# Optimization experiments

Measured on AMD Instinct MI355X. Metric: run time of the kernel, lower is better.

Reference implementation:

```python
import jax, jax.numpy as jnp
import numpy as np

D_MODEL = 2048
NUM_HEADS = 16
D_K = D_MODEL // NUM_HEADS
B, S = 2, 2048


def setup_inputs() -> dict:
    key = jax.random.key(0)
    ks = jax.random.split(key, 9)
    sc = 1.0 / np.sqrt(D_MODEL)
    x = jax.random.normal(ks[0], (B, S, D_MODEL), dtype=jnp.float32)
    # broadcastable causal mask [1,1,S,S]; mask==0 positions get -inf
    mask = jnp.tril(jnp.ones((S, S), dtype=jnp.int32))[None, None]
    wq = jax.random.normal(ks[1], (D_MODEL, D_MODEL), dtype=jnp.float32) * sc
    bq = jax.random.normal(ks[2], (D_MODEL,), dtype=jnp.float32) * 0.01
    wk = jax.random.normal(ks[3], (D_MODEL, D_MODEL), dtype=jnp.float32) * sc
    bk = jax.random.normal(ks[4], (D_MODEL,), dtype=jnp.float32) * 0.01
    wv = jax.random.normal(ks[5], (D_MODEL, D_MODEL), dtype=jnp.float32) * sc
    bv = jax.random.normal(ks[6], (D_MODEL,), dtype=jnp.float32) * 0.01
    wo = jax.random.normal(ks[7], (D_MODEL, D_MODEL), dtype=jnp.float32) * sc
    bo = jax.random.normal(ks[8], (D_MODEL,), dtype=jnp.float32) * 0.01
    return {"x": x, "wq": wq, "bq": bq, "wk": wk, "bk": bk,
            "wv": wv, "bv": bv, "wo": wo, "bo": bo, "mask": mask}


def reference(x, wq, bq, wk, bk, wv, bv, wo, bo, mask):
    b, s, _ = x.shape
    # nn.Linear computes x @ W.T + b; weights stored [out, in]
    def proj(w, bias):
        y = jnp.einsum('bsd,ed->bse', x, w) + bias
        return y.reshape(b, s, NUM_HEADS, D_K).transpose(0, 2, 1, 3)  # [b,h,s,dk]
    q = proj(wq, bq)
    k = proj(wk, bk)
    v = proj(wv, bv)
    scores = jnp.einsum('bhid,bhjd->bhij', q, k) / jnp.sqrt(jnp.float32(D_K))
    scores = jnp.where(mask == 0, -jnp.inf, scores)
    attn = jax.nn.softmax(scores, axis=-1)  # dropout p=0.0 -> identity
    out = jnp.einsum('bhij,bhjd->bhid', attn, v)
    out = out.transpose(0, 2, 1, 3).reshape(b, s, D_MODEL)
    return jnp.einsum('bsd,ed->bse', out, wo) + bo
```

## Files before the change

### kernel.cpp

```cpp
#include <hip/hip_runtime.h>
#include <cstdint>
#include <cstddef>

typedef __attribute__((ext_vector_type(8))) short bf16x8;
typedef __attribute__((ext_vector_type(8))) unsigned short u16x8;
typedef __attribute__((ext_vector_type(4))) unsigned short u16x4;
typedef __attribute__((ext_vector_type(4))) float f32x4;

#define MFMA16(A, B, C) __builtin_amdgcn_mfma_f32_16x16x32_bf16((A), (B), (C), 0, 0, 0)

__device__ __forceinline__ unsigned short f2bf(float f) {
  unsigned u = __builtin_bit_cast(unsigned, f);
  u += 0x7FFFu + ((u >> 16) & 1u);
  return (unsigned short)(u >> 16);
}

__device__ __forceinline__ void gload_lds16(const void* gsrc, void* ldst) {
  __builtin_amdgcn_global_load_lds(
      (const __attribute__((address_space(1))) unsigned int*)gsrc,
      (__attribute__((address_space(3))) unsigned int*)ldst,
      16, 0, 0);
}

__global__ __launch_bounds__(256) void cvt_all(
    const float* __restrict__ sx, const float* __restrict__ s1,
    const float* __restrict__ s2, const float* __restrict__ s3,
    const float* __restrict__ s4,
    unsigned short* __restrict__ dx, unsigned short* __restrict__ d1,
    unsigned short* __restrict__ d2, unsigned short* __restrict__ d3,
    unsigned short* __restrict__ d4) {
  const int y = blockIdx.y;
  const float* src;
  unsigned short* dst;
  if (y == 0)      { src = sx;               dst = dx; }
  else if (y == 1) { src = sx + (1u << 22);  dst = dx + (1u << 22); }
  else if (y == 2) { src = s1; dst = d1; }
  else if (y == 3) { src = s2; dst = d2; }
  else if (y == 4) { src = s3; dst = d3; }
  else             { src = s4; dst = d4; }
  const size_t i = ((size_t)blockIdx.x * 256 + threadIdx.x) * 4;
  f32x4 v = *(const f32x4*)(src + i);
  u16x4 o;
  o[0] = f2bf(v[0]); o[1] = f2bf(v[1]); o[2] = f2bf(v[2]); o[3] = f2bf(v[3]);
  *(u16x4*)(dst + i) = o;
}

template <int MODE>
__device__ __forceinline__ void gemm_tile(const unsigned short* __restrict__ A,
                                          const unsigned short* __restrict__ W,
                                          const float* __restrict__ bias,
                                          void* __restrict__ C,
                                          int bx, int by) {
  constexpr int K = 2048, N = 2048;
  __shared__ unsigned short lA[128 * 32];
  __shared__ unsigned short lB[128 * 32];
  const int tid = threadIdx.x;
  const int lane = tid & 63;
  const int w = tid >> 6;
  const int g = lane >> 4;
  const int l15 = lane & 15;
  const int wr = w >> 1, wc = w & 1;
  const int m0 = by * 128, n0 = bx * 128;

  f32x4 acc[4][4];
#pragma unroll
  for (int i = 0; i < 4; ++i)
#pragma unroll
    for (int j = 0; j < 4; ++j) acc[i][j] = f32x4{0.f, 0.f, 0.f, 0.f};

  for (int kt = 0; kt < K / 32; ++kt) {
    __syncthreads();
    const int kb = kt * 32;
#pragma unroll
    for (int it = 0; it < 2; ++it) {
      const int f = it * 256 + tid;
      const int r = f >> 2, s = f & 3;
      char* dA = (char*)lA + (it * 256 + w * 64) * 16;
      char* dB = (char*)lB + (it * 256 + w * 64) * 16;
      gload_lds16(A + (size_t)(m0 + r) * K + kb + s * 8, dA);
      gload_lds16(W + (size_t)(n0 + r) * K + kb + s * 8, dB);
    }
    __syncthreads();
    bf16x8 af[4], bfr[4];
#pragma unroll
    for (int mi = 0; mi < 4; ++mi)
      af[mi] = *(const bf16x8*)&lA[(wr * 64 + mi * 16 + l15) * 32 + g * 8];
#pragma unroll
    for (int ni = 0; ni < 4; ++ni)
      bfr[ni] = *(const bf16x8*)&lB[(wc * 64 + ni * 16 + l15) * 32 + g * 8];
#pragma unroll
    for (int mi = 0; mi < 4; ++mi)
#pragma unroll
      for (int ni = 0; ni < 4; ++ni)
        acc[mi][ni] = MFMA16(af[mi], bfr[ni], acc[mi][ni]);
  }

#pragma unroll
  for (int ni = 0; ni < 4; ++ni) {
    const int n = n0 + wc * 64 + ni * 16 + l15;
    const float bval = bias[n];
#pragma unroll
    for (int mi = 0; mi < 4; ++mi) {
      const int mb = m0 + wr * 64 + mi * 16 + g * 4;
#pragma unroll
      for (int r = 0; r < 4; ++r) {
        const int m = mb + r;
        const float fv = acc[mi][ni][r] + bval;
        if (MODE == 0) {
          ((float*)C)[(size_t)m * N + n] = fv;
        } else {
          const int bb = m >> 11, ss = m & 2047, hh = n >> 7, dk = n & 127;
          ((unsigned short*)C)[(((size_t)(bb * 16 + hh) * 2048) + ss) * 128 + dk] =
              f2bf(fv);
        }
      }
    }
  }
}

__global__ __launch_bounds__(256) void gemm_qkv(
    const unsigned short* __restrict__ x,
    const unsigned short* __restrict__ wq, const float* __restrict__ bq,
    const unsigned short* __restrict__ wk, const float* __restrict__ bk,
    const unsigned short* __restrict__ wv, const float* __restrict__ bv,
    unsigned short* __restrict__ qo, unsigned short* __restrict__ ko,
    unsigned short* __restrict__ vo) {
  const int z = blockIdx.z;
  const unsigned short* W = (z == 0) ? wq : (z == 1) ? wk : wv;
  const float* B = (z == 0) ? bq : (z == 1) ? bk : bv;
  unsigned short* O = (z == 0) ? qo : (z == 1) ? ko : vo;
  gemm_tile<1>(x, W, B, O, blockIdx.x, blockIdx.y);
}

__global__ __launch_bounds__(256) void gemm_out(
    const unsigned short* __restrict__ A, const unsigned short* __restrict__ wo,
    const float* __restrict__ bo, float* __restrict__ C) {
  gemm_tile<0>(A, wo, bo, C, blockIdx.x, blockIdx.y);
}

__global__ __launch_bounds__(256, 2) void attn_fwd(
    const unsigned short* __restrict__ Q, const unsigned short* __restrict__ K,
    const unsigned short* __restrict__ V, unsigned short* __restrict__ O) {
  __shared__ unsigned short lK[2][64 * 128];
  __shared__ unsigned short lV[128 * 72];
  __shared__ unsigned short lP[4][32 * 72];
  const int tid = threadIdx.x;
  const int lane = tid & 63;
  const int w = tid >> 6;
  const int g = lane >> 4;
  const int l15 = lane & 15;
  const int bx = blockIdx.x;
  const int bh = blockIdx.y;
  const int qb = (bh >= 16) ? (15 - bx) : bx;
  const int nt = 2 * qb + 2;
  const size_t head_off = (size_t)bh * 2048 * 128;
  const unsigned short* Qh = Q + head_off;
  const unsigned short* Kh = K + head_off;
  const unsigned short* Vh = V + head_off;

  bf16x8 qf[2][4];
#pragma unroll
  for (int mi = 0; mi < 2; ++mi) {
    const int row = qb * 128 + w * 32 + mi * 16 + l15;
#pragma unroll
    for (int ks = 0; ks < 4; ++ks) {
      const int s = ks * 4 + g;
      qf[mi][ks] = *(const bf16x8*)(Qh + (size_t)row * 128 + s * 8);
    }
  }

  const int vj0 = (tid & 31) * 2;
  const int vd0 = (tid >> 5) * 16;
  u16x8 vr[4];

  auto stageK = [&](int t, int buf) {
#pragma unroll
    for (int it = 0; it < 4; ++it) {
      const int f = it * 256 + tid;
      const int r = f >> 4, s = f & 15;
      const int sc = s ^ (r & 7);
      gload_lds16(Kh + (size_t)(t * 64 + r) * 128 + sc * 8,
                  (char*)&lK[buf][0] + (it * 256 + w * 64) * 16);
    }
  };
  auto loadV = [&](int t) {
    const unsigned short* vp = Vh + (size_t)(t * 64 + vj0) * 128 + vd0;
    vr[0] = *(const u16x8*)(vp);
    vr[1] = *(const u16x8*)(vp + 8);
    vr[2] = *(const u16x8*)(vp + 128);
    vr[3] = *(const u16x8*)(vp + 136);
  };
  auto writeV = [&]() {
#pragma unroll
    for (int dd = 0; dd < 8; ++dd) {
      unsigned pk0 = (unsigned)vr[0][dd] | ((unsigned)vr[2][dd] << 16);
      unsigned pk1 = (unsigned)vr[1][dd] | ((unsigned)vr[3][dd] << 16);
      *(unsigned*)&lV[(vd0 + dd) * 72 + vj0] = pk0;
      *(unsigned*)&lV[(vd0 + 8 + dd) * 72 + vj0] = pk1;
    }
  };

  loadV(0);
  stageK(0, 0);
  writeV();
  __syncthreads();

  f32x4 acc_o[2][8];
#pragma unroll
  for (int mi = 0; mi < 2; ++mi)
#pragma unroll
    for (int i = 0; i < 8; ++i) acc_o[mi][i] = f32x4{0.f, 0.f, 0.f, 0.f};
  float mrun[2], lrun[2];
#pragma unroll
  for (int mi = 0; mi < 2; ++mi) { mrun[mi] = -__builtin_inff(); lrun[mi] = 0.f; }

  const float SL2E = 0.12751744f;
  const int qrow0 = qb * 128 + w * 32;

  int cur = 0;
  for (int t = 0; t < nt; ++t) {
    const int kv0 = t * 64;
    const bool pre = (t + 1 < nt);
    if (pre) { loadV(t + 1); stageK(t + 1, cur ^ 1); }

    const bool active = (kv0 <= qrow0 + 31);
    if (active) {
      const unsigned short* lKc = &lK[cur][0];
      f32x4 sacc[4][2];
#pragma unroll
      for (int jb = 0; jb < 4; ++jb) {
        sacc[jb][0] = f32x4{0.f, 0.f, 0.f, 0.f};
        sacc[jb][1] = f32x4{0.f, 0.f, 0.f, 0.f};
      }
      __builtin_amdgcn_s_setprio(1);
#pragma unroll
      for (int jb = 0; jb < 4; ++jb) {
        const int r = jb * 16 + l15;
#pragma unroll
        for (int ks = 0; ks < 4; ++ks) {
          const int s = ks * 4 + g;
          bf16x8 kf = *(const bf16x8*)&lKc[r * 128 + (s ^ (r & 7)) * 8];
          sacc[jb][0] = MFMA16(kf, qf[0][ks], sacc[jb][0]);
          sacc[jb][1] = MFMA16(kf, qf[1][ks], sacc[jb][1]);
        }
      }
      __builtin_amdgcn_s_setprio(0);

      const bool need_mask = (kv0 + 63 >= qrow0);
      float psc_l[2];
#pragma unroll
      for (int mi = 0; mi < 2; ++mi) {
        const int icol = qrow0 + mi * 16 + l15;
        f32x4 pe[4];
#pragma unroll
        for (int jb = 0; jb < 4; ++jb) {
#pragma unroll
          for (int rr = 0; rr < 4; ++rr) {
            float tv = sacc[jb][mi][rr] * SL2E;
            if (need_mask && (kv0 + jb * 16 + g * 4 + rr > icol))
              tv = -__builtin_inff();
            pe[jb][rr] = tv;
          }
        }
        f32x4 m4 = f32x4{fmaxf(fmaxf(pe[0][0], pe[1][0]), fmaxf(pe[2][0], pe[3][0])),
                         fmaxf(fmaxf(pe[0][1], pe[1][1]), fmaxf(pe[2][1], pe[3][1])),
                         fmaxf(fmaxf(pe[0][2], pe[1][2]), fmaxf(pe[2][2], pe[3][2])),
                         fmaxf(fmaxf(pe[0][3], pe[1][3]), fmaxf(pe[2][3], pe[3][3]))};
        float mx = fmaxf(fmaxf(m4[0], m4[1]), fmaxf(m4[2], m4[3]));
        mx = fmaxf(mx, __shfl_xor(mx, 16));
        mx = fmaxf(mx, __shfl_xor(mx, 32));
        const float mnew = fmaxf(mrun[mi], mx);
        psc_l[mi] = exp2f(mrun[mi] - mnew);
        mrun[mi] = mnew;
        float rs = 0.f;
#pragma unroll
        for (int jb = 0; jb < 4; ++jb) {
#pragma unroll
          for (int rr = 0; rr < 4; ++rr) {
            const float e = exp2f(pe[jb][rr] - mnew);
            pe[jb][rr] = e;
            rs += e;
          }
        }
        rs += __shfl_xor(rs, 16);
        rs += __shfl_xor(rs, 32);
        lrun[mi] = lrun[mi] * psc_l[mi] + rs;
#pragma unroll
        for (int jb = 0; jb < 4; ++jb)
#pragma unroll
          for (int rr = 0; rr < 4; ++rr)
            lP[w][(mi * 16 + l15) * 72 + jb * 16 + g * 4 + rr] = f2bf(pe[jb][rr]);
      }
      __builtin_amdgcn_sched_barrier(0);

      float psc_pv[2][4];
#pragma unroll
      for (int mi = 0; mi < 2; ++mi)
#pragma unroll
        for (int r = 0; r < 4; ++r)
          psc_pv[mi][r] = __shfl(psc_l[mi], g * 4 + r);
#pragma unroll
      for (int mi = 0; mi < 2; ++mi)
#pragma unroll
        for (int nb = 0; nb < 8; ++nb)
#pragma unroll
          for (int r = 0; r < 4; ++r) acc_o[mi][nb][r] *= psc_pv[mi][r];

      bf16x8 pa[2][2];
#pragma unroll
      for (int mi = 0; mi < 2; ++mi)
#pragma unroll
        for (int h = 0; h < 2; ++h)
          pa[mi][h] = *(const bf16x8*)&lP[w][(mi * 16 + l15) * 72 + h * 32 + g * 8];
      __builtin_amdgcn_s_setprio(1);
#pragma unroll
      for (int nb = 0; nb < 8; ++nb) {
        const int vrow = nb * 16 + l15;
#pragma unroll
        for (int h = 0; h < 2; ++h) {
          bf16x8 vf = *(const bf16x8*)&lV[vrow * 72 + h * 32 + g * 8];
          acc_o[0][nb] = MFMA16(pa[0][h], vf, acc_o[0][nb]);
          acc_o[1][nb] = MFMA16(pa[1][h], vf, acc_o[1][nb]);
        }
      }
      __builtin_amdgcn_s_setprio(0);
    }

    __syncthreads();
    if (pre) writeV();
    __syncthreads();
    cur ^= 1;
  }

  const int b = bh >> 4, hh = bh & 15;
  float linv[2][4];
#pragma unroll
  for (int mi = 0; mi < 2; ++mi)
#pragma unroll
    for (int r = 0; r < 4; ++r)
      linv[mi][r] = 1.0f / __shfl(lrun[mi], g * 4 + r);
#pragma unroll
  for (int mi = 0; mi < 2; ++mi)
#pragma unroll
    for (int nb = 0; nb < 8; ++nb)
#pragma unroll
      for (int r = 0; r < 4; ++r) {
        const int i = qb * 128 + w * 32 + mi * 16 + g * 4 + r;
        const float o = acc_o[mi][nb][r] * linv[mi][r];
        O[((size_t)(b * 2048 + i)) * 2048 + hh * 128 + nb * 16 + l15] = f2bf(o);
      }
}

extern "C" void kernel_launch(void* const* d_in, const int* in_sizes, int n_in,
                              void* d_out, int out_size, void* d_ws, size_t ws_size,
                              hipStream_t stream) {
  const float* x  = (const float*)d_in[0];
  const float* wq = (const float*)d_in[1];
  const float* bq = (const float*)d_in[2];
  const float* wk = (const float*)d_in[3];
  const float* bk = (const float*)d_in[4];
  const float* wv = (const float*)d_in[5];
  const float* bv = (const float*)d_in[6];
  const float* wo = (const float*)d_in[7];
  const float* bo = (const float*)d_in[8];

  const size_t NX = (size_t)2 * 2048 * 2048;
  const size_t NW = (size_t)2048 * 2048;
  const size_t need = (NX + 4 * NW + 3 * NX) * sizeof(unsigned short);
  if (ws_size < need) return;
  unsigned short* xbf  = (unsigned short*)d_ws;
  unsigned short* wqb  = xbf + NX;
  unsigned short* wkb  = wqb + NW;
  unsigned short* wvb  = wkb + NW;
  unsigned short* wob  = wvb + NW;
  unsigned short* qbuf = wob + NW;
  unsigned short* kbuf = qbuf + NX;
  unsigned short* vbuf = kbuf + NX;
  unsigned short* aobuf = xbf;

  cvt_all<<<dim3(4096, 6), 256, 0, stream>>>(x, wq, wk, wv, wo,
                                             xbf, wqb, wkb, wvb, wob);
  gemm_qkv<<<dim3(16, 32, 3), 256, 0, stream>>>(xbf, wqb, bq, wkb, bk, wvb, bv,
                                                qbuf, kbuf, vbuf);
  attn_fwd<<<dim3(16, 32), 256, 0, stream>>>(qbuf, kbuf, vbuf, aobuf);
  gemm_out<<<dim3(16, 32), 256, 0, stream>>>(aobuf, wob, bo, (float*)d_out);
}
```

Before: 298.7 us.

## Rewrite projection GEMMs as 8-wave 256x128 tiles with triple-buffered swizzled LDS

The QKV and output projection GEMMs now use 512-thread blocks computing 256x128 tiles with a K-step of 64. Global-to-LDS loads are triple-buffered and issued two steps ahead, split between the two MFMA phases and gated by explicit vmcnt waits and barriers. LDS rows use an XOR swizzle to avoid bank conflicts, and s_setprio raises priority around the MFMA bursts. The aim is to overlap memory latency with matrix math and cut per-iteration barrier overhead. In exchange, LDS use per block grows to about 144 KB and the grid has half as many blocks.

```diff
diff --git a/kernel.cpp b/kernel.cpp
--- a/kernel.cpp
+++ b/kernel.cpp
@@ -46,21 +46,43 @@
 }
 
 template <int MODE>
-__device__ __forceinline__ void gemm_tile(const unsigned short* __restrict__ A,
-                                          const unsigned short* __restrict__ W,
-                                          const float* __restrict__ bias,
-                                          void* __restrict__ C,
-                                          int bx, int by) {
+__device__ __forceinline__ void gemm8_tile(const unsigned short* __restrict__ A,
+                                           const unsigned short* __restrict__ W,
+                                           const float* __restrict__ bias,
+                                           void* __restrict__ C,
+                                           int bx, int by) {
   constexpr int K = 2048, N = 2048;
-  __shared__ unsigned short lA[128 * 32];
-  __shared__ unsigned short lB[128 * 32];
+  constexpr int NT = K / 64;
+  __shared__ unsigned short lA[3][256 * 64];
+  __shared__ unsigned short lB[3][128 * 64];
   const int tid = threadIdx.x;
   const int lane = tid & 63;
   const int w = tid >> 6;
   const int g = lane >> 4;
   const int l15 = lane & 15;
-  const int wr = w >> 1, wc = w & 1;
-  const int m0 = by * 128, n0 = bx * 128;
+  const int wm = w >> 1, wn = w & 1;
+  const int m0 = by * 256, n0 = bx * 128;
+
+  auto stageA = [&](int kt, int buf) {
+    const int kb = kt * 64;
+#pragma unroll
+    for (int it = 0; it < 4; ++it) {
+      const int f = it * 512 + tid;
+      const int r = f >> 3, s = f & 7;
+      gload_lds16(A + (size_t)(m0 + r) * K + kb + ((s * 8) ^ ((r & 7) << 3)),
+                  (char*)&lA[buf][0] + (it * 512 + w * 64) * 16);
+    }
+  };
+  auto stageB = [&](int kt, int buf) {
+    const int kb = kt * 64;
+#pragma unroll
+    for (int it = 0; it < 2; ++it) {
+      const int f = it * 512 + tid;
+      const int r = f >> 3, s = f & 7;
+      gload_lds16(W + (size_t)(n0 + r) * K + kb + ((s * 8) ^ ((r & 7) << 3)),
+                  (char*)&lB[buf][0] + (it * 512 + w * 64) * 16);
+    }
+  };
 
   f32x4 acc[4][4];
 #pragma unroll
@@ -68,40 +90,82 @@
 #pragma unroll
     for (int j = 0; j < 4; ++j) acc[i][j] = f32x4{0.f, 0.f, 0.f, 0.f};
 
-  for (int kt = 0; kt < K / 32; ++kt) {
-    __syncthreads();
-    const int kb = kt * 32;
-#pragma unroll
-    for (int it = 0; it < 2; ++it) {
-      const int f = it * 256 + tid;
-      const int r = f >> 2, s = f & 3;
-      char* dA = (char*)lA + (it * 256 + w * 64) * 16;
-      char* dB = (char*)lB + (it * 256 + w * 64) * 16;
-      gload_lds16(A + (size_t)(m0 + r) * K + kb + s * 8, dA);
-      gload_lds16(W + (size_t)(n0 + r) * K + kb + s * 8, dB);
-    }
-    __syncthreads();
-    bf16x8 af[4], bfr[4];
-#pragma unroll
-    for (int mi = 0; mi < 4; ++mi)
-      af[mi] = *(const bf16x8*)&lA[(wr * 64 + mi * 16 + l15) * 32 + g * 8];
-#pragma unroll
-    for (int ni = 0; ni < 4; ++ni)
-      bfr[ni] = *(const bf16x8*)&lB[(wc * 64 + ni * 16 + l15) * 32 + g * 8];
-#pragma unroll
-    for (int mi = 0; mi < 4; ++mi)
-#pragma unroll
-      for (int ni = 0; ni < 4; ++ni)
-        acc[mi][ni] = MFMA16(af[mi], bfr[ni], acc[mi][ni]);
+  stageA(0, 0); stageB(0, 0);
+  stageA(1, 1); stageB(1, 1);
+  asm volatile("s_waitcnt vmcnt(6)" ::: "memory");
+  __builtin_amdgcn_s_barrier();
+  __builtin_amdgcn_sched_barrier(0);
+
+  int cur = 0, nxt = 2;
+  for (int kt = 0; kt < NT; ++kt) {
+    const unsigned short* As = &lA[cur][0];
+    const unsigned short* Bs = &lB[cur][0];
+    bf16x8 bfr[4][2], af[2][2];
+#pragma unroll
+    for (int ni = 0; ni < 4; ++ni) {
+      const int rb = wn * 64 + ni * 16 + l15;
+#pragma unroll
+      for (int kh = 0; kh < 2; ++kh)
+        bfr[ni][kh] =
+            *(const bf16x8*)&Bs[rb * 64 + ((kh * 32 + g * 8) ^ ((rb & 7) << 3))];
+    }
+#pragma unroll
+    for (int mi = 0; mi < 2; ++mi) {
+      const int ra = wm * 64 + mi * 16 + l15;
+#pragma unroll
+      for (int kh = 0; kh < 2; ++kh)
+        af[mi][kh] =
+            *(const bf16x8*)&As[ra * 64 + ((kh * 32 + g * 8) ^ ((ra & 7) << 3))];
+    }
+    if (kt + 2 < NT) stageA(kt + 2, nxt);
+    __builtin_amdgcn_s_barrier();
+    __builtin_amdgcn_sched_barrier(0);
+    __builtin_amdgcn_s_setprio(1);
+#pragma unroll
+    for (int kh = 0; kh < 2; ++kh)
+#pragma unroll
+      for (int mi = 0; mi < 2; ++mi)
+#pragma unroll
+        for (int ni = 0; ni < 4; ++ni)
+          acc[mi][ni] = MFMA16(af[mi][kh], bfr[ni][kh], acc[mi][ni]);
+    __builtin_amdgcn_s_setprio(0);
+    __builtin_amdgcn_s_barrier();
+    __builtin_amdgcn_sched_barrier(0);
+#pragma unroll
+    for (int mi = 0; mi < 2; ++mi) {
+      const int ra = wm * 64 + (mi + 2) * 16 + l15;
+#pragma unroll
+      for (int kh = 0; kh < 2; ++kh)
+        af[mi][kh] =
+            *(const bf16x8*)&As[ra * 64 + ((kh * 32 + g * 8) ^ ((ra & 7) << 3))];
+    }
+    if (kt + 2 < NT) stageB(kt + 2, nxt);
+    __builtin_amdgcn_s_barrier();
+    __builtin_amdgcn_sched_barrier(0);
+    __builtin_amdgcn_s_setprio(1);
+#pragma unroll
+    for (int kh = 0; kh < 2; ++kh)
+#pragma unroll
+      for (int mi = 0; mi < 2; ++mi)
+#pragma unroll
+        for (int ni = 0; ni < 4; ++ni)
+          acc[mi + 2][ni] = MFMA16(af[mi][kh], bfr[ni][kh], acc[mi + 2][ni]);
+    __builtin_amdgcn_s_setprio(0);
+    if (kt < NT - 2)       asm volatile("s_waitcnt vmcnt(6)" ::: "memory");
+    else if (kt == NT - 2) asm volatile("s_waitcnt vmcnt(0)" ::: "memory");
+    __builtin_amdgcn_s_barrier();
+    __builtin_amdgcn_sched_barrier(0);
+    cur = (cur == 2) ? 0 : cur + 1;
+    nxt = (nxt == 2) ? 0 : nxt + 1;
   }
 
 #pragma unroll
   for (int ni = 0; ni < 4; ++ni) {
-    const int n = n0 + wc * 64 + ni * 16 + l15;
+    const int n = n0 + wn * 64 + ni * 16 + l15;
     const float bval = bias[n];
 #pragma unroll
     for (int mi = 0; mi < 4; ++mi) {
-      const int mb = m0 + wr * 64 + mi * 16 + g * 4;
+      const int mb = m0 + wm * 64 + mi * 16 + g * 4;
 #pragma unroll
       for (int r = 0; r < 4; ++r) {
         const int m = mb + r;
@@ -118,7 +182,7 @@
   }
 }
 
-__global__ __launch_bounds__(256) void gemm_qkv(
+__global__ __launch_bounds__(512, 2) void gemm_qkv(
     const unsigned short* __restrict__ x,
     const unsigned short* __restrict__ wq, const float* __restrict__ bq,
     const unsigned short* __restrict__ wk, const float* __restrict__ bk,
@@ -129,13 +193,13 @@
   const unsigned short* W = (z == 0) ? wq : (z == 1) ? wk : wv;
   const float* B = (z == 0) ? bq : (z == 1) ? bk : bv;
   unsigned short* O = (z == 0) ? qo : (z == 1) ? ko : vo;
-  gemm_tile<1>(x, W, B, O, blockIdx.x, blockIdx.y);
-}
-
-__global__ __launch_bounds__(256) void gemm_out(
+  gemm8_tile<1>(x, W, B, O, blockIdx.x, blockIdx.y);
+}
+
+__global__ __launch_bounds__(512, 2) void gemm_out(
     const unsigned short* __restrict__ A, const unsigned short* __restrict__ wo,
     const float* __restrict__ bo, float* __restrict__ C) {
-  gemm_tile<0>(A, wo, bo, C, blockIdx.x, blockIdx.y);
+  gemm8_tile<0>(A, wo, bo, C, blockIdx.x, blockIdx.y);
 }
 
 __global__ __launch_bounds__(256, 2) void attn_fwd(
@@ -380,8 +444,8 @@
 
   cvt_all<<<dim3(4096, 6), 256, 0, stream>>>(x, wq, wk, wv, wo,
                                              xbf, wqb, wkb, wvb, wob);
-  gemm_qkv<<<dim3(16, 32, 3), 256, 0, stream>>>(xbf, wqb, bq, wkb, bk, wvb, bv,
+  gemm_qkv<<<dim3(16, 16, 3), 512, 0, stream>>>(xbf, wqb, bq, wkb, bk, wvb, bv,
                                                 qbuf, kbuf, vbuf);
   attn_fwd<<<dim3(16, 32), 256, 0, stream>>>(qbuf, kbuf, vbuf, aobuf);
-  gemm_out<<<dim3(16, 32), 256, 0, stream>>>(aobuf, wob, bo, (float*)d_out);
-}
+  gemm_out<<<dim3(16, 16), 512, 0, stream>>>(aobuf, wob, bo, (float*)d_out);
+}
```

Result: faster. 292.0 us (-2.2%).
